# Optimization experiments

Hardware: AMD Instinct MI355X
Metric: run time of the kernel (lower is better)

Reference implementation:

```python
import jax, jax.numpy as jnp
import numpy as np


def setup_inputs() -> dict:
    key = jax.random.key(0)
    k1, k2 = jax.random.split(key)
    B, C = 2097152, 10
    p = jax.random.uniform(k1, (B, C, 1), dtype=jnp.float32)
    q = jax.random.uniform(k2, (B, C, 1), dtype=jnp.float32)
    return {"p": p, "q": q, "r": 2}


def reference(p, q, r):
    # p, q: [B, C, 1]. Original: per-sample EMD = (mean_i |cumsum_{<=i}(p-q)|^r)^(1/r),
    # then averaged over the batch.
    diff = (p - q)[..., 0]                      # [B, C]
    cdf_diff = jnp.cumsum(diff, axis=1)         # [B, C] prefix sums
    per_sample = jnp.mean(jnp.abs(cdf_diff) ** r, axis=1) ** (1.0 / r)  # [B]
    return jnp.mean(per_sample)
```

## Files before the change

kernel.cpp:

```cpp
#include <hip/hip_runtime.h>
#include <math.h>


constexpr int C = 10;
constexpr int BLOCK = 256;

__device__ __forceinline__ float block_reduce_sum(float v) {
    #pragma unroll
    for (int off = 32; off > 0; off >>= 1)
        v += __shfl_down(v, off, 64);
    __shared__ float smem[BLOCK / 64];
    const int lane = threadIdx.x & 63;
    const int wid  = threadIdx.x >> 6;
    if (lane == 0) smem[wid] = v;
    __syncthreads();
    float s = 0.0f;
    if (threadIdx.x == 0) {
        #pragma unroll
        for (int w = 0; w < BLOCK / 64; ++w) s += smem[w];
    }
    return s;
}

__global__ __launch_bounds__(BLOCK) void emd_partial(
    const float* __restrict__ p, const float* __restrict__ q,
    const int* __restrict__ rptr, float* __restrict__ partial, int B)
{
    const int tid = blockIdx.x * blockDim.x + threadIdx.x;
    const int nth = gridDim.x * blockDim.x;
    const int r   = rptr[0];
    const int npairs = B >> 1;

    float local = 0.0f;

    if (r == 2) {
        for (int pi = tid; pi < npairs; pi += nth) {
            const float4* p4 = reinterpret_cast<const float4*>(p) + (size_t)pi * 5;
            const float4* q4 = reinterpret_cast<const float4*>(q) + (size_t)pi * 5;
            float d[2 * C];
            #pragma unroll
            for (int k = 0; k < 5; ++k) {
                float4 a = p4[k];
                float4 b = q4[k];
                d[4*k+0] = a.x - b.x;
                d[4*k+1] = a.y - b.y;
                d[4*k+2] = a.z - b.z;
                d[4*k+3] = a.w - b.w;
            }
            #pragma unroll
            for (int s = 0; s < 2; ++s) {
                float cum = 0.0f, acc = 0.0f;
                #pragma unroll
                for (int c = 0; c < C; ++c) {
                    cum += d[s * C + c];
                    acc += cum * cum;
                }
                local += sqrtf(acc * (1.0f / C));
            }
        }
    } else {
        const float rf = (float)r;
        const float rinv = 1.0f / rf;
        for (int pi = tid; pi < npairs; pi += nth) {
            const float4* p4 = reinterpret_cast<const float4*>(p) + (size_t)pi * 5;
            const float4* q4 = reinterpret_cast<const float4*>(q) + (size_t)pi * 5;
            float d[2 * C];
            #pragma unroll
            for (int k = 0; k < 5; ++k) {
                float4 a = p4[k];
                float4 b = q4[k];
                d[4*k+0] = a.x - b.x;
                d[4*k+1] = a.y - b.y;
                d[4*k+2] = a.z - b.z;
                d[4*k+3] = a.w - b.w;
            }
            #pragma unroll
            for (int s = 0; s < 2; ++s) {
                float cum = 0.0f, acc = 0.0f;
                #pragma unroll
                for (int c = 0; c < C; ++c) {
                    cum += d[s * C + c];
                    acc += powf(fabsf(cum), rf);
                }
                local += powf(acc * (1.0f / C), rinv);
            }
        }
    }

    if ((B & 1) && tid == 0) {
        const size_t base = (size_t)(B - 1) * C;
        float cum = 0.0f, acc = 0.0f;
        for (int c = 0; c < C; ++c) {
            cum += p[base + c] - q[base + c];
            acc += (r == 2) ? cum * cum : powf(fabsf(cum), (float)r);
        }
        local += (r == 2) ? sqrtf(acc * (1.0f / C))
                          : powf(acc * (1.0f / C), 1.0f / (float)r);
    }

    float s = block_reduce_sum(local);
    if (threadIdx.x == 0) partial[blockIdx.x] = s;
}

__global__ __launch_bounds__(BLOCK) void emd_reduce(
    const float* __restrict__ partial, int n, float* __restrict__ out, float invB)
{
    float local = 0.0f;
    for (int i = threadIdx.x; i < n; i += BLOCK) local += partial[i];
    float s = block_reduce_sum(local);
    if (threadIdx.x == 0) out[0] = s * invB;
}

extern "C" void kernel_launch(void* const* d_in, const int* in_sizes, int n_in,
                              void* d_out, int out_size, void* d_ws, size_t ws_size,
                              hipStream_t stream) {
    const float* p = (const float*)d_in[0];
    const float* q = (const float*)d_in[1];
    const int*   r = (const int*)d_in[2];
    float* out     = (float*)d_out;
    float* partial = (float*)d_ws;

    const int B = in_sizes[0] / C;

    int nblocks = 2048;
    const int max_ws_blocks = (int)(ws_size / sizeof(float));
    if (nblocks > max_ws_blocks) nblocks = max_ws_blocks;
    if (nblocks < 1) nblocks = 1;

    emd_partial<<<nblocks, BLOCK, 0, stream>>>(p, q, r, partial, B);
    emd_reduce<<<1, BLOCK, 0, stream>>>(partial, nblocks, out, 1.0f / (float)B);
}
```

Measured before the change: 32.67 us.

## Stage coalesced float4 tiles through LDS for per-pair EMD computation

Each block now loads a 256-pair tile of p and q with fully coalesced float4 loads (consecutive threads read consecutive vectors), stores it in shared memory, and then each thread reads its own 5 float4s from LDS. The goal is to replace the strided 80-byte-per-thread global reads, which coalesce poorly, with contiguous accesses. The grid is also halved to 1024 blocks. In exchange it adds two __syncthreads per tile, LDS bank traffic from stride-5 float4 reads, and less overlap of loads with compute.

Measured after the change: 32.65 us. Within noise of the previous version (-0.1%).

```diff
diff --git a/kernel.cpp b/kernel.cpp
--- a/kernel.cpp
+++ b/kernel.cpp
@@ -4,6 +4,9 @@
 
 constexpr int C = 10;
 constexpr int BLOCK = 256;
+constexpr int TILE = 256;
+constexpr int F4T = TILE * 5;
+constexpr int NBLOCKS = 1024;
 
 __device__ __forceinline__ float block_reduce_sum(float v) {
     #pragma unroll
@@ -22,72 +25,101 @@
     return s;
 }
 
+__device__ __forceinline__ float pair_emd(const float* d, int r) {
+    float res = 0.0f;
+    if (r == 2) {
+        #pragma unroll
+        for (int s = 0; s < 2; ++s) {
+            float cum = 0.0f, acc = 0.0f;
+            #pragma unroll
+            for (int c = 0; c < C; ++c) {
+                cum += d[s * C + c];
+                acc += cum * cum;
+            }
+            res += sqrtf(acc * (1.0f / C));
+        }
+    } else {
+        const float rf = (float)r, rinv = 1.0f / rf;
+        #pragma unroll
+        for (int s = 0; s < 2; ++s) {
+            float cum = 0.0f, acc = 0.0f;
+            #pragma unroll
+            for (int c = 0; c < C; ++c) {
+                cum += d[s * C + c];
+                acc += powf(fabsf(cum), rf);
+            }
+            res += powf(acc * (1.0f / C), rinv);
+        }
+    }
+    return res;
+}
+
 __global__ __launch_bounds__(BLOCK) void emd_partial(
     const float* __restrict__ p, const float* __restrict__ q,
     const int* __restrict__ rptr, float* __restrict__ partial, int B)
 {
-    const int tid = blockIdx.x * blockDim.x + threadIdx.x;
-    const int nth = gridDim.x * blockDim.x;
+    __shared__ float4 sp[F4T];
+    __shared__ float4 sq[F4T];
+
+    const int tid = threadIdx.x;
     const int r   = rptr[0];
     const int npairs = B >> 1;
+    const int ntiles = npairs / TILE;
+    const int rem    = npairs - ntiles * TILE;
+
+    const float4* p4 = reinterpret_cast<const float4*>(p);
+    const float4* q4 = reinterpret_cast<const float4*>(q);
 
     float local = 0.0f;
 
-    if (r == 2) {
-        for (int pi = tid; pi < npairs; pi += nth) {
-            const float4* p4 = reinterpret_cast<const float4*>(p) + (size_t)pi * 5;
-            const float4* q4 = reinterpret_cast<const float4*>(q) + (size_t)pi * 5;
-            float d[2 * C];
-            #pragma unroll
-            for (int k = 0; k < 5; ++k) {
-                float4 a = p4[k];
-                float4 b = q4[k];
-                d[4*k+0] = a.x - b.x;
-                d[4*k+1] = a.y - b.y;
-                d[4*k+2] = a.z - b.z;
-                d[4*k+3] = a.w - b.w;
-            }
-            #pragma unroll
-            for (int s = 0; s < 2; ++s) {
-                float cum = 0.0f, acc = 0.0f;
-                #pragma unroll
-                for (int c = 0; c < C; ++c) {
-                    cum += d[s * C + c];
-                    acc += cum * cum;
-                }
-                local += sqrtf(acc * (1.0f / C));
-            }
+    for (int t = blockIdx.x; t < ntiles; t += gridDim.x) {
+        const size_t base = (size_t)t * F4T;
+
+        float4 rp[5], rq[5];
+        #pragma unroll
+        for (int k = 0; k < 5; ++k) {
+            rp[k] = p4[base + tid + BLOCK * k];
+            rq[k] = q4[base + tid + BLOCK * k];
         }
-    } else {
-        const float rf = (float)r;
-        const float rinv = 1.0f / rf;
-        for (int pi = tid; pi < npairs; pi += nth) {
-            const float4* p4 = reinterpret_cast<const float4*>(p) + (size_t)pi * 5;
-            const float4* q4 = reinterpret_cast<const float4*>(q) + (size_t)pi * 5;
-            float d[2 * C];
-            #pragma unroll
-            for (int k = 0; k < 5; ++k) {
-                float4 a = p4[k];
-                float4 b = q4[k];
-                d[4*k+0] = a.x - b.x;
-                d[4*k+1] = a.y - b.y;
-                d[4*k+2] = a.z - b.z;
-                d[4*k+3] = a.w - b.w;
-            }
-            #pragma unroll
-            for (int s = 0; s < 2; ++s) {
-                float cum = 0.0f, acc = 0.0f;
-                #pragma unroll
-                for (int c = 0; c < C; ++c) {
-                    cum += d[s * C + c];
-                    acc += powf(fabsf(cum), rf);
-                }
-                local += powf(acc * (1.0f / C), rinv);
-            }
+        #pragma unroll
+        for (int k = 0; k < 5; ++k) {
+            sp[tid + BLOCK * k] = rp[k];
+            sq[tid + BLOCK * k] = rq[k];
         }
+        __syncthreads();
+
+        const float4* spp = &sp[tid * 5];
+        const float4* sqq = &sq[tid * 5];
+        float d[2 * C];
+        #pragma unroll
+        for (int j = 0; j < 5; ++j) {
+            float4 a = spp[j];
+            float4 b = sqq[j];
+            d[4*j+0] = a.x - b.x;
+            d[4*j+1] = a.y - b.y;
+            d[4*j+2] = a.z - b.z;
+            d[4*j+3] = a.w - b.w;
+        }
+        local += pair_emd(d, r);
+        __syncthreads();
     }
 
-    if ((B & 1) && tid == 0) {
+    if (rem && blockIdx.x == 0 && tid < rem) {
+        const size_t pi = (size_t)ntiles * TILE + tid;
+        float d[2 * C];
+        #pragma unroll
+        for (int k = 0; k < 5; ++k) {
+            float4 a = p4[pi * 5 + k];
+            float4 b = q4[pi * 5 + k];
+            d[4*k+0] = a.x - b.x;
+            d[4*k+1] = a.y - b.y;
+            d[4*k+2] = a.z - b.z;
+            d[4*k+3] = a.w - b.w;
+        }
+        local += pair_emd(d, r);
+    }
+
+    if ((B & 1) && blockIdx.x == 0 && tid == 0) {
         const size_t base = (size_t)(B - 1) * C;
         float cum = 0.0f, acc = 0.0f;
         for (int c = 0; c < C; ++c) {
@@ -99,7 +131,7 @@
     }
 
     float s = block_reduce_sum(local);
-    if (threadIdx.x == 0) partial[blockIdx.x] = s;
+    if (tid == 0) partial[blockIdx.x] = s;
 }
 
 __global__ __launch_bounds__(BLOCK) void emd_reduce(
@@ -122,7 +154,7 @@
 
     const int B = in_sizes[0] / C;
 
-    int nblocks = 2048;
+    int nblocks = NBLOCKS;
     const int max_ws_blocks = (int)(ws_size / sizeof(float));
     if (nblocks > max_ws_blocks) nblocks = max_ws_blocks;
     if (nblocks < 1) nblocks = 1;
```
